# Optimization experiments

Hardware: AMD Instinct MI355X
Metric: run time of the kernel (lower is better)

Reference implementation:

```python
import jax, jax.numpy as jnp
import numpy as np

N_NODES = 100000
N_EDGES = 3200000
N_GRAPHS = 256


def setup_inputs() -> dict:
    key = jax.random.key(0)
    ks = jax.random.split(key, 8)
    x = jax.random.normal(ks[0], (N_NODES, 13), dtype=jnp.float32)
    edge_index = jax.random.randint(ks[1], (2, N_EDGES), 0, N_NODES, dtype=jnp.int64)
    batch = jnp.sort(jax.random.randint(ks[2], (N_NODES,), 0, N_GRAPHS, dtype=jnp.int64))
    W1 = jax.random.normal(ks[3], (13, 64), dtype=jnp.float32) * 0.1
    b1 = jnp.zeros((64,), dtype=jnp.float32)
    W2 = jax.random.normal(ks[4], (64, 64), dtype=jnp.float32) * 0.1
    b2 = jnp.zeros((64,), dtype=jnp.float32)
    W3 = jax.random.normal(ks[5], (64, 32), dtype=jnp.float32) * 0.1
    b3 = jnp.zeros((32,), dtype=jnp.float32)
    return {"x": x, "edge_index": edge_index, "batch": batch,
            "W1": W1, "b1": b1, "W2": W2, "b2": b2, "W3": W3, "b3": b3}


def _gcn_norm(edge_index, num_nodes):
    # PyG GCNConv default: add self-loops, symmetric D^-1/2 (A+I) D^-1/2 normalization.
    loops = jnp.arange(num_nodes, dtype=edge_index.dtype)
    src = jnp.concatenate([edge_index[0], loops])
    dst = jnp.concatenate([edge_index[1], loops])
    ones = jnp.ones(src.shape[0], dtype=jnp.float32)
    deg = jax.ops.segment_sum(ones, dst, num_segments=num_nodes)
    dinv = jnp.where(deg > 0, jax.lax.rsqrt(deg), 0.0)
    norm = dinv[src] * dinv[dst]  # [E+N]
    return src, dst, norm


def _gcn_conv(h, W, b, src, dst, norm, num_nodes):
    h = h @ W                                   # [N, out]
    msg = h[src] * norm[:, None]                # gather + scale, [E+N, out]
    out = jax.ops.segment_sum(msg, dst, num_segments=num_nodes)  # scatter-add
    return out + b


def reference(x, edge_index, batch, W1, b1, W2, b2, W3, b3):
    n = x.shape[0]
    src, dst, norm = _gcn_norm(edge_index, n)
    h = jax.nn.relu(_gcn_conv(x, W1, b1, src, dst, norm, n))
    h = jax.nn.relu(_gcn_conv(h, W2, b2, src, dst, norm, n))
    h = _gcn_conv(h, W3, b3, src, dst, norm, n)
    # global_mean_pool over graphs
    sums = jax.ops.segment_sum(h, batch, num_segments=N_GRAPHS)
    counts = jax.ops.segment_sum(jnp.ones((n,), jnp.float32), batch, num_segments=N_GRAPHS)
    return sums / jnp.maximum(counts, 1.0)[:, None]
```

## Files before the change

### kernel.cpp

```cpp
#include <hip/hip_runtime.h>
#include <hip/hip_fp16.h>

constexpr int NN = 100000;
constexpr int NE = 3200000;
constexpr int NG = 256;
constexpr int NCB = 196;
constexpr int TILE = 4096;
constexpr int EPT = TILE / 256;
constexpr int CAP = 17408;
constexpr int L1_BLOCKS = 1024;
constexpr int L1_WAVES = L1_BLOCKS * 4;

__global__ void k_zero_i(int* __restrict__ p, int n) {
  int i = blockIdx.x * blockDim.x + threadIdx.x;
  if (i < n) p[i] = 0;
}

__global__ void k_msplit(const int* __restrict__ src, const int* __restrict__ dst,
                         int* __restrict__ gcursor, int* __restrict__ pairs, int E) {
  constexpr int NT = 256;
  __shared__ int hist[NCB], lbase[NCB], lcur[NCB], gwrite[NCB];
  __shared__ int staged[TILE];
  __shared__ unsigned char sbid[TILE];
  __shared__ int stot;
  const int tid = threadIdx.x;
  const int e0 = blockIdx.x * TILE;
  for (int i = tid; i < NCB; i += NT) { hist[i] = 0; lcur[i] = 0; }
  __syncthreads();
  int4 ls[EPT / 4], ld[EPT / 4];
  bool valid[EPT / 4];
#pragma unroll
  for (int j = 0; j < EPT / 4; ++j) {
    int e = e0 + j * (NT * 4) + tid * 4;
    valid[j] = (e < E);
    if (valid[j]) {
      ls[j] = *(const int4*)(src + e);
      ld[j] = *(const int4*)(dst + e);
      atomicAdd(&hist[ld[j].x >> 9], 1);
      atomicAdd(&hist[ld[j].y >> 9], 1);
      atomicAdd(&hist[ld[j].z >> 9], 1);
      atomicAdd(&hist[ld[j].w >> 9], 1);
    }
  }
  __syncthreads();
  if (tid == 0) {
    int run = 0;
    for (int c = 0; c < NCB; ++c) { lbase[c] = run; run += hist[c]; }
    stot = run;
  }
  __syncthreads();
  for (int c = tid; c < NCB; c += NT) {
    int cnt = hist[c];
    if (cnt > 0) {
      int g = atomicAdd(&gcursor[c], cnt);
      gwrite[c] = c * CAP + g;
    }
  }
  __syncthreads();
#pragma unroll
  for (int j = 0; j < EPT / 4; ++j) {
    if (valid[j]) {
      int ss[4] = {ls[j].x, ls[j].y, ls[j].z, ls[j].w};
      int dd[4] = {ld[j].x, ld[j].y, ld[j].z, ld[j].w};
#pragma unroll
      for (int q = 0; q < 4; ++q) {
        int c = dd[q] >> 9;
        int pos = lbase[c] + atomicAdd(&lcur[c], 1);
        staged[pos] = ss[q] | ((dd[q] & 511) << 17);
        sbid[pos] = (unsigned char)c;
      }
    }
  }
  __syncthreads();
  const int total = stot;
  for (int i = tid; i < total; i += NT) {
    int c = sbid[i];
    pairs[gwrite[c] + (i - lbase[c])] = staged[i];
  }
}

__global__ void k_brow(const int* __restrict__ pairs, const int* __restrict__ gcursor,
                       int* __restrict__ rowstart, float* __restrict__ dinv,
                       int* __restrict__ csr_src) {
  __shared__ int deg[512], pre[512], cur[512];
  __shared__ int s[256];
  const int cb = blockIdx.x;
  const int n0 = cb << 9;
  const int tid = threadIdx.x;
  s[tid] = (tid < NCB) ? gcursor[tid] : 0;
  __syncthreads();
  for (int o = 1; o < 256; o <<= 1) {
    int v = s[tid];
    int u = (tid >= o) ? s[tid - o] : 0;
    __syncthreads();
    s[tid] = v + u;
    __syncthreads();
  }
  const int e0 = (cb == 0) ? 0 : s[cb - 1];
  const int cnt = gcursor[cb];
  const int p0 = cb * CAP;
  __syncthreads();
  for (int i = tid; i < 512; i += 256) { deg[i] = 0; cur[i] = 0; }
  __syncthreads();
  for (int e = tid; e < cnt; e += 256) atomicAdd(&deg[pairs[p0 + e] >> 17], 1);
  __syncthreads();
  int d0 = deg[2 * tid], d1 = deg[2 * tid + 1];
  s[tid] = d0 + d1;
  __syncthreads();
  for (int o = 1; o < 256; o <<= 1) {
    int v = s[tid];
    int u = (tid >= o) ? s[tid - o] : 0;
    __syncthreads();
    s[tid] = v + u;
    __syncthreads();
  }
  int p2 = (tid == 0) ? 0 : s[tid - 1];
  pre[2 * tid] = p2;
  pre[2 * tid + 1] = p2 + d0;
  __syncthreads();
  for (int i = tid; i < 512; i += 256) {
    int n = n0 + i;
    if (n < NN) {
      rowstart[n] = e0 + pre[i];
      dinv[n] = rsqrtf((float)(deg[i] + 1));
    }
  }
  if (cb == NCB - 1 && tid == 0) rowstart[NN] = NE;
  for (int e = tid; e < cnt; e += 256) {
    int w = pairs[p0 + e];
    int dl = w >> 17;
    int p = e0 + pre[dl] + atomicAdd(&cur[dl], 1);
    csr_src[p] = w & 0x1FFFF;
  }
}

__global__ void k_xs(const float* __restrict__ x, const float* __restrict__ dinv,
                     __half* __restrict__ xs) {
  int i = blockIdx.x * blockDim.x + threadIdx.x;
  if (i < NN * 16) {
    int v = i >> 4, f = i & 15;
    float val = (f < 13) ? x[v * 13 + f] * dinv[v] : 0.0f;
    xs[i] = __float2half_rn(val);
  }
}

__global__ void __launch_bounds__(256, 4) k_l1fused(
    const __half* __restrict__ xs, const int* __restrict__ rowstart,
    const int* __restrict__ csr_src, const float* __restrict__ dinv,
    const float* __restrict__ W1, const float* __restrict__ b1,
    const float* __restrict__ W2, __half* __restrict__ t2) {
  __shared__ float W1s[13 * 64];
  __shared__ float B1s[64];
  __shared__ float aggs[4][16];
  __shared__ float h1s[4][64];
  __shared__ int lidx[4][64];
  const int tid = threadIdx.x;
  for (int i = tid; i < 13 * 64; i += 256) W1s[i] = W1[i];
  if (tid < 64) B1s[tid] = b1[tid];
  const int wv = tid >> 6;
  const int lane = tid & 63;
  const int c4 = lane & 15, kh = lane >> 4;
  float w2r[16][4];
#pragma unroll
  for (int i = 0; i < 16; ++i) {
    float4 v = *(const float4*)(W2 + (kh * 16 + i) * 64 + c4 * 4);
    w2r[i][0] = v.x; w2r[i][1] = v.y; w2r[i][2] = v.z; w2r[i][3] = v.w;
  }
  __syncthreads();
  const int fp = lane & 7;
  const int es = lane >> 3;
  const __half2* x2 = (const __half2*)xs;
  for (int node = blockIdx.x * 4 + wv; node < NN; node += L1_WAVES) {
    const int r0 = rowstart[node], r1 = rowstart[node + 1];
    float ax = 0.0f, ay = 0.0f;
    if (es == 0) {
      float2 sf = __half22float2(x2[node * 8 + fp]);
      ax = sf.x; ay = sf.y;
    }
    for (int base = r0; base < r1; base += 64) {
      const int nc = min(64, r1 - base);
      lidx[wv][lane] = (base + lane < r1) ? csr_src[base + lane] : 0;
      int i = es;
      for (; i + 24 < nc; i += 32) {
        int s0 = lidx[wv][i], s1 = lidx[wv][i + 8], s2 = lidx[wv][i + 16], s3 = lidx[wv][i + 24];
        float2 v0 = __half22float2(x2[s0 * 8 + fp]);
        float2 v1 = __half22float2(x2[s1 * 8 + fp]);
        float2 v2 = __half22float2(x2[s2 * 8 + fp]);
        float2 v3 = __half22float2(x2[s3 * 8 + fp]);
        ax += (v0.x + v1.x) + (v2.x + v3.x);
        ay += (v0.y + v1.y) + (v2.y + v3.y);
      }
      for (; i < nc; i += 8) {
        int s = lidx[wv][i];
        float2 v = __half22float2(x2[s * 8 + fp]);
        ax += v.x; ay += v.y;
      }
    }
    ax += __shfl_xor(ax, 32); ay += __shfl_xor(ay, 32);
    ax += __shfl_xor(ax, 16); ay += __shfl_xor(ay, 16);
    ax += __shfl_xor(ax, 8);  ay += __shfl_xor(ay, 8);
    const float di = dinv[node];
    if (lane < 8) {
      aggs[wv][2 * fp]     = ax * di;
      aggs[wv][2 * fp + 1] = ay * di;
    }
    float acc = B1s[lane];
#pragma unroll
    for (int k = 0; k < 13; ++k) acc += aggs[wv][k] * W1s[k * 64 + lane];
    h1s[wv][lane] = fmaxf(acc, 0.0f);
    float a0 = 0.0f, a1 = 0.0f, a2 = 0.0f, a3 = 0.0f;
#pragma unroll
    for (int i = 0; i < 16; ++i) {
      float hb = h1s[wv][kh * 16 + i];
      a0 += hb * w2r[i][0];
      a1 += hb * w2r[i][1];
      a2 += hb * w2r[i][2];
      a3 += hb * w2r[i][3];
    }
    a0 += __shfl_xor(a0, 16); a0 += __shfl_xor(a0, 32);
    a1 += __shfl_xor(a1, 16); a1 += __shfl_xor(a1, 32);
    a2 += __shfl_xor(a2, 16); a2 += __shfl_xor(a2, 32);
    a3 += __shfl_xor(a3, 16); a3 += __shfl_xor(a3, 32);
    if (kh == 0) {
      __half2* o = (__half2*)t2;
      o[node * 32 + c4 * 2]     = __floats2half2_rn(a0 * di, a1 * di);
      o[node * 32 + c4 * 2 + 1] = __floats2half2_rn(a2 * di, a3 * di);
    }
  }
}

__global__ void __launch_bounds__(256) k_gather64m(
    const __half* __restrict__ t, const int* __restrict__ rowstart,
    const int* __restrict__ csr_src, const float* __restrict__ dinv,
    const float* __restrict__ b2, const float* __restrict__ W3,
    __half* __restrict__ t3) {
  __shared__ float W3s[64 * 32];
  __shared__ float h2s[4][64];
  __shared__ int lidx[4][64];
  const int tid = threadIdx.x;
  for (int i = tid; i < 64 * 32; i += 256) W3s[i] = W3[i];
  __syncthreads();
  const int w = tid >> 6;
  const int lane = tid & 63;
  const int node = blockIdx.x * 4 + w;
  const int fp = lane & 31;
  const int es = lane >> 5;
  const __half2* t2 = (const __half2*)t;
  const int r0 = rowstart[node], r1 = rowstart[node + 1];
  float ax = 0.0f, ay = 0.0f;
  if (es == 0) {
    float2 sf = __half22float2(t2[node * 32 + fp]);
    ax = sf.x; ay = sf.y;
  }
  for (int base = r0; base < r1; base += 64) {
    const int nc = min(64, r1 - base);
    lidx[w][lane] = (base + lane < r1) ? csr_src[base + lane] : 0;
    int i = es;
    for (; i + 14 < nc; i += 16) {
      int s0 = lidx[w][i],      s1 = lidx[w][i + 2],  s2 = lidx[w][i + 4],  s3 = lidx[w][i + 6];
      int s4 = lidx[w][i + 8],  s5 = lidx[w][i + 10], s6 = lidx[w][i + 12], s7 = lidx[w][i + 14];
      float2 v0 = __half22float2(t2[s0 * 32 + fp]);
      float2 v1 = __half22float2(t2[s1 * 32 + fp]);
      float2 v2 = __half22float2(t2[s2 * 32 + fp]);
      float2 v3 = __half22float2(t2[s3 * 32 + fp]);
      float2 v4 = __half22float2(t2[s4 * 32 + fp]);
      float2 v5 = __half22float2(t2[s5 * 32 + fp]);
      float2 v6 = __half22float2(t2[s6 * 32 + fp]);
      float2 v7 = __half22float2(t2[s7 * 32 + fp]);
      ax += ((v0.x + v1.x) + (v2.x + v3.x)) + ((v4.x + v5.x) + (v6.x + v7.x));
      ay += ((v0.y + v1.y) + (v2.y + v3.y)) + ((v4.y + v5.y) + (v6.y + v7.y));
    }
    for (; i < nc; i += 2) {
      int s = lidx[w][i];
      float2 v = __half22float2(t2[s * 32 + fp]);
      ax += v.x; ay += v.y;
    }
  }
  ax += __shfl_xor(ax, 32); ay += __shfl_xor(ay, 32);
  const float di = dinv[node];
  if (es == 0) {
    float2 bb = ((const float2*)b2)[fp];
    h2s[w][2 * fp]     = fmaxf(ax * di + bb.x, 0.0f);
    h2s[w][2 * fp + 1] = fmaxf(ay * di + bb.y, 0.0f);
  }
  const int j = lane & 31, kh = lane >> 5;
  float p = 0.0f;
#pragma unroll
  for (int k2 = 0; k2 < 32; ++k2) {
    int k = kh * 32 + k2;
    p += h2s[w][k] * W3s[k * 32 + j];
  }
  p += __shfl_xor(p, 32);
  if (lane < 32) t3[node * 32 + j] = __float2half_rn(p * di);
}

__global__ void k_gather32w(const __half* __restrict__ t, const int* __restrict__ rowstart,
                            const int* __restrict__ csr_src,
                            const float* __restrict__ dinv, const float* __restrict__ b,
                            __half* __restrict__ h3) {
  __shared__ int lidx[4][64];
  const int wv = threadIdx.x >> 6;
  const int node = (blockIdx.x * blockDim.x + threadIdx.x) >> 6;
  const int lane = threadIdx.x & 63;
  const int fp = lane & 15;
  const int es = lane >> 4;
  const __half2* t2 = (const __half2*)t;
  const int r0 = rowstart[node], r1 = rowstart[node + 1];
  float ax = 0.0f, ay = 0.0f;
  if (es == 0) {
    float2 sf = __half22float2(t2[node * 16 + fp]);
    ax = sf.x; ay = sf.y;
  }
  for (int base = r0; base < r1; base += 64) {
    const int nc = min(64, r1 - base);
    lidx[wv][lane] = (base + lane < r1) ? csr_src[base + lane] : 0;
    int i = es;
    for (; i + 28 < nc; i += 32) {
      int s0 = lidx[wv][i],      s1 = lidx[wv][i + 4],  s2 = lidx[wv][i + 8],  s3 = lidx[wv][i + 12];
      int s4 = lidx[wv][i + 16], s5 = lidx[wv][i + 20], s6 = lidx[wv][i + 24], s7 = lidx[wv][i + 28];
      float2 v0 = __half22float2(t2[s0 * 16 + fp]);
      float2 v1 = __half22float2(t2[s1 * 16 + fp]);
      float2 v2 = __half22float2(t2[s2 * 16 + fp]);
      float2 v3 = __half22float2(t2[s3 * 16 + fp]);
      float2 v4 = __half22float2(t2[s4 * 16 + fp]);
      float2 v5 = __half22float2(t2[s5 * 16 + fp]);
      float2 v6 = __half22float2(t2[s6 * 16 + fp]);
      float2 v7 = __half22float2(t2[s7 * 16 + fp]);
      ax += ((v0.x + v1.x) + (v2.x + v3.x)) + ((v4.x + v5.x) + (v6.x + v7.x));
      ay += ((v0.y + v1.y) + (v2.y + v3.y)) + ((v4.y + v5.y) + (v6.y + v7.y));
    }
    for (; i < nc; i += 4) {
      int s = lidx[wv][i];
      float2 v = __half22float2(t2[s * 16 + fp]);
      ax += v.x; ay += v.y;
    }
  }
  ax += __shfl_xor(ax, 32); ay += __shfl_xor(ay, 32);
  ax += __shfl_xor(ax, 16); ay += __shfl_xor(ay, 16);
  if (lane < 16) {
    const float di = dinv[node];
    float2 bb = ((const float2*)b)[fp];
    ((__half2*)h3)[node * 16 + fp] = __floats2half2_rn(ax * di + bb.x, ay * di + bb.y);
  }
}

__global__ void k_pool(const __half* __restrict__ h3, const int* __restrict__ batch,
                       float* __restrict__ out) {
  const int g = blockIdx.x;
  int lo = 0, hi = NN;
  while (lo < hi) { int m = (lo + hi) >> 1; if (batch[m] < g) lo = m + 1; else hi = m; }
  const int a = lo;
  lo = 0; hi = NN;
  while (lo < hi) { int m = (lo + hi) >> 1; if (batch[m] < g + 1) lo = m + 1; else hi = m; }
  const int bEnd = lo;
  const int tid = threadIdx.x;
  const int nl = tid >> 4, f = tid & 15;
  const __half2* h2p = (const __half2*)h3;
  float ax = 0.0f, ay = 0.0f;
  for (int n = a + nl; n < bEnd; n += 16) {
    float2 v = __half22float2(h2p[n * 16 + f]);
    ax += v.x; ay += v.y;
  }
  __shared__ float redx[16][16], redy[16][16];
  redx[nl][f] = ax; redy[nl][f] = ay;
  __syncthreads();
  if (tid < 16) {
    float sx = 0.0f, sy = 0.0f;
#pragma unroll
    for (int i = 0; i < 16; ++i) { sx += redx[i][tid]; sy += redy[i][tid]; }
    float inv = 1.0f / fmaxf((float)(bEnd - a), 1.0f);
    ((float2*)out)[g * 16 + tid] = make_float2(sx * inv, sy * inv);
  }
}

extern "C" void kernel_launch(void* const* d_in, const int* in_sizes, int n_in,
                              void* d_out, int out_size, void* d_ws, size_t ws_size,
                              hipStream_t stream) {
  const float* x  = (const float*)d_in[0];
  const int*   ei = (const int*)d_in[1];
  const int* batch = (const int*)d_in[2];
  const float* W1 = (const float*)d_in[3];
  const float* b1 = (const float*)d_in[4];
  const float* W2 = (const float*)d_in[5];
  const float* b2 = (const float*)d_in[6];
  const float* W3 = (const float*)d_in[7];
  const float* b3 = (const float*)d_in[8];
  float* out = (float*)d_out;

  const int* src = ei;
  const int* dst = ei + NE;

  float* ws = (float*)d_ws;
  float* dinv     = ws;
  int*   gcursor  = (int*)(ws + 100352);
  int*   rowstart = (int*)(ws + 100944);
  int*   csr_src  = (int*)(ws + 201056);
  float* bufT     = ws + 3401056;
  float* bufH     = ws + 9801056;
  int*    pairs = (int*)bufT;
  __half* t2    = (__half*)bufT;
  __half* h3    = (__half*)(bufT + 1600000);
  __half* xs    = (__half*)bufH;
  __half* t3    = (__half*)bufH;

  const int B = 256;
  auto cdiv = [](int a, int b) { return (a + b - 1) / b; };

  k_zero_i<<<1, B, 0, stream>>>(gcursor, NCB);
  k_msplit<<<cdiv(NE, TILE), B, 0, stream>>>(src, dst, gcursor, pairs, NE);
  k_brow<<<NCB, B, 0, stream>>>(pairs, gcursor, rowstart, dinv, csr_src);

  k_xs<<<cdiv(NN * 16, B), B, 0, stream>>>(x, dinv, xs);
  k_l1fused<<<L1_BLOCKS, B, 0, stream>>>(xs, rowstart, csr_src, dinv, W1, b1, W2, t2);

  k_gather64m<<<NN / 4, B, 0, stream>>>(t2, rowstart, csr_src, dinv, b2, W3, t3);

  k_gather32w<<<cdiv(NN * 64, B), B, 0, stream>>>(t3, rowstart, csr_src, dinv, b3, h3);
  k_pool<<<NG, B, 0, stream>>>(h3, batch, out);
}
```

Measured before the change: 295.2 us.

## Use finer 256-node destination buckets for CSR build and parallelize bucket scan

Halves the destination bucket width used for the CSR construction from 512 to 256 nodes. This roughly doubles the number of buckets and k_brow blocks (391 instead of 196), so the row-building pass gets enough blocks to spread across the GPU's compute units. The serial single-thread prefix sum over bucket histograms in k_msplit is replaced with a block-wide parallel scan. Per-bucket capacity and buffer offsets are adjusted to match, which adds more global cursor atomics and more scattered pair writes per tile.

```diff
diff --git a/kernel.cpp b/kernel.cpp
--- a/kernel.cpp
+++ b/kernel.cpp
@@ -4,10 +4,10 @@
 constexpr int NN = 100000;
 constexpr int NE = 3200000;
 constexpr int NG = 256;
-constexpr int NCB = 196;
+constexpr int NCB = 391;
 constexpr int TILE = 4096;
 constexpr int EPT = TILE / 256;
-constexpr int CAP = 17408;
+constexpr int CAP = 9216;
 constexpr int L1_BLOCKS = 1024;
 constexpr int L1_WAVES = L1_BLOCKS * 4;
 
@@ -19,13 +19,14 @@
 __global__ void k_msplit(const int* __restrict__ src, const int* __restrict__ dst,
                          int* __restrict__ gcursor, int* __restrict__ pairs, int E) {
   constexpr int NT = 256;
-  __shared__ int hist[NCB], lbase[NCB], lcur[NCB], gwrite[NCB];
+  __shared__ int hist[512], lbase[512], lcur[NCB], gwrite[NCB];
+  __shared__ unsigned short sbid[TILE];
   __shared__ int staged[TILE];
-  __shared__ unsigned char sbid[TILE];
-  __shared__ int stot;
+  __shared__ int s[256];
   const int tid = threadIdx.x;
   const int e0 = blockIdx.x * TILE;
-  for (int i = tid; i < NCB; i += NT) { hist[i] = 0; lcur[i] = 0; }
+  for (int i = tid; i < 512; i += NT) hist[i] = 0;
+  for (int i = tid; i < NCB; i += NT) lcur[i] = 0;
   __syncthreads();
   int4 ls[EPT / 4], ld[EPT / 4];
   bool valid[EPT / 4];
@@ -36,18 +37,26 @@
     if (valid[j]) {
       ls[j] = *(const int4*)(src + e);
       ld[j] = *(const int4*)(dst + e);
-      atomicAdd(&hist[ld[j].x >> 9], 1);
-      atomicAdd(&hist[ld[j].y >> 9], 1);
-      atomicAdd(&hist[ld[j].z >> 9], 1);
-      atomicAdd(&hist[ld[j].w >> 9], 1);
-    }
-  }
-  __syncthreads();
-  if (tid == 0) {
-    int run = 0;
-    for (int c = 0; c < NCB; ++c) { lbase[c] = run; run += hist[c]; }
-    stot = run;
-  }
+      atomicAdd(&hist[ld[j].x >> 8], 1);
+      atomicAdd(&hist[ld[j].y >> 8], 1);
+      atomicAdd(&hist[ld[j].z >> 8], 1);
+      atomicAdd(&hist[ld[j].w >> 8], 1);
+    }
+  }
+  __syncthreads();
+  int h0 = hist[2 * tid], h1 = hist[2 * tid + 1];
+  s[tid] = h0 + h1;
+  __syncthreads();
+  for (int o = 1; o < 256; o <<= 1) {
+    int v = s[tid];
+    int u = (tid >= o) ? s[tid - o] : 0;
+    __syncthreads();
+    s[tid] = v + u;
+    __syncthreads();
+  }
+  int p2 = (tid == 0) ? 0 : s[tid - 1];
+  lbase[2 * tid] = p2;
+  lbase[2 * tid + 1] = p2 + h0;
   __syncthreads();
   for (int c = tid; c < NCB; c += NT) {
     int cnt = hist[c];
@@ -64,15 +73,15 @@
       int dd[4] = {ld[j].x, ld[j].y, ld[j].z, ld[j].w};
 #pragma unroll
       for (int q = 0; q < 4; ++q) {
-        int c = dd[q] >> 9;
+        int c = dd[q] >> 8;
         int pos = lbase[c] + atomicAdd(&lcur[c], 1);
-        staged[pos] = ss[q] | ((dd[q] & 511) << 17);
-        sbid[pos] = (unsigned char)c;
+        staged[pos] = ss[q] | ((dd[q] & 255) << 17);
+        sbid[pos] = (unsigned short)c;
       }
     }
   }
   __syncthreads();
-  const int total = stot;
+  const int total = (e0 + TILE <= E) ? TILE : (E - e0);
   for (int i = tid; i < total; i += NT) {
     int c = sbid[i];
     pairs[gwrite[c] + (i - lbase[c])] = staged[i];
@@ -82,12 +91,15 @@
 __global__ void k_brow(const int* __restrict__ pairs, const int* __restrict__ gcursor,
                        int* __restrict__ rowstart, float* __restrict__ dinv,
                        int* __restrict__ csr_src) {
-  __shared__ int deg[512], pre[512], cur[512];
+  __shared__ int deg[256], pre[256], cur[256];
+  __shared__ int cbaseL[512];
   __shared__ int s[256];
   const int cb = blockIdx.x;
-  const int n0 = cb << 9;
+  const int n0 = cb << 8;
   const int tid = threadIdx.x;
-  s[tid] = (tid < NCB) ? gcursor[tid] : 0;
+  int g0 = (2 * tid < NCB) ? gcursor[2 * tid] : 0;
+  int g1 = (2 * tid + 1 < NCB) ? gcursor[2 * tid + 1] : 0;
+  s[tid] = g0 + g1;
   __syncthreads();
   for (int o = 1; o < 256; o <<= 1) {
     int v = s[tid];
@@ -96,16 +108,20 @@
     s[tid] = v + u;
     __syncthreads();
   }
-  const int e0 = (cb == 0) ? 0 : s[cb - 1];
+  int p2 = (tid == 0) ? 0 : s[tid - 1];
+  cbaseL[2 * tid] = p2;
+  cbaseL[2 * tid + 1] = p2 + g0;
+  __syncthreads();
+  const int e0 = cbaseL[cb];
   const int cnt = gcursor[cb];
   const int p0 = cb * CAP;
-  __syncthreads();
-  for (int i = tid; i < 512; i += 256) { deg[i] = 0; cur[i] = 0; }
-  __syncthreads();
-  for (int e = tid; e < cnt; e += 256) atomicAdd(&deg[pairs[p0 + e] >> 17], 1);
-  __syncthreads();
-  int d0 = deg[2 * tid], d1 = deg[2 * tid + 1];
-  s[tid] = d0 + d1;
+  deg[tid] = 0;
+  cur[tid] = 0;
+  __syncthreads();
+  for (int e = tid; e < cnt; e += 256) atomicAdd(&deg[(pairs[p0 + e] >> 17) & 255], 1);
+  __syncthreads();
+  int d = deg[tid];
+  s[tid] = d;
   __syncthreads();
   for (int o = 1; o < 256; o <<= 1) {
     int v = s[tid];
@@ -114,21 +130,17 @@
     s[tid] = v + u;
     __syncthreads();
   }
-  int p2 = (tid == 0) ? 0 : s[tid - 1];
-  pre[2 * tid] = p2;
-  pre[2 * tid + 1] = p2 + d0;
-  __syncthreads();
-  for (int i = tid; i < 512; i += 256) {
-    int n = n0 + i;
-    if (n < NN) {
-      rowstart[n] = e0 + pre[i];
-      dinv[n] = rsqrtf((float)(deg[i] + 1));
-    }
+  pre[tid] = (tid == 0) ? 0 : s[tid - 1];
+  __syncthreads();
+  const int n = n0 + tid;
+  if (n < NN) {
+    rowstart[n] = e0 + pre[tid];
+    dinv[n] = rsqrtf((float)(d + 1));
   }
   if (cb == NCB - 1 && tid == 0) rowstart[NN] = NE;
   for (int e = tid; e < cnt; e += 256) {
     int w = pairs[p0 + e];
-    int dl = w >> 17;
+    int dl = (w >> 17) & 255;
     int p = e0 + pre[dl] + atomicAdd(&cur[dl], 1);
     csr_src[p] = w & 0x1FFFF;
   }
@@ -399,14 +411,14 @@
   float* bufH     = ws + 9801056;
   int*    pairs = (int*)bufT;
   __half* t2    = (__half*)bufT;
-  __half* h3    = (__half*)(bufT + 1600000);
+  __half* h3    = (__half*)(bufT + 1801728);
   __half* xs    = (__half*)bufH;
   __half* t3    = (__half*)bufH;
 
   const int B = 256;
   auto cdiv = [](int a, int b) { return (a + b - 1) / b; };
 
-  k_zero_i<<<1, B, 0, stream>>>(gcursor, NCB);
+  k_zero_i<<<2, B, 0, stream>>>(gcursor, NCB);
   k_msplit<<<cdiv(NE, TILE), B, 0, stream>>>(src, dst, gcursor, pairs, NE);
   k_brow<<<NCB, B, 0, stream>>>(pairs, gcursor, rowstart, dinv, csr_src);
 
```

Result: faster. 282.8 us (-4.2%).
